# Optimization experiments

Measured on AMD Instinct MI355X. Metric: run time of the kernel, lower is better.

## Reference

```python
import jax, jax.numpy as jnp
import numpy as np

H = 64  # hidden size

def setup_inputs() -> dict:
    key = jax.random.key(0)
    ks = jax.random.split(key, 7)
    B, T = 256, 5000
    s = 1.0 / np.sqrt(H)  # PyTorch LSTM init scale
    return {
        "x":    jax.random.normal(ks[0], (B, T), dtype=jnp.float32),
        "W_ih": jax.random.uniform(ks[1], (4 * H, 1), jnp.float32, -s, s),
        "W_hh": jax.random.uniform(ks[2], (4 * H, H), jnp.float32, -s, s),
        "b_ih": jax.random.uniform(ks[3], (4 * H,), jnp.float32, -s, s),
        "b_hh": jax.random.uniform(ks[4], (4 * H,), jnp.float32, -s, s),
        "W_fc": jax.random.uniform(ks[5], (128, H), jnp.float32, -s, s),
        "b_fc": jax.random.uniform(ks[6], (128,), jnp.float32, -s, s),
    }

def _lstm_last_hidden(x, W_ih, W_hh, b_ih, b_hh):
    # x: [B, T]; returns last hidden state h_T: [B, H]
    B, T = x.shape
    # input projection for all timesteps at once: [B, T, 4H]
    # (input_size == 1, so this is an outer product with W_ih[:, 0])
    x_proj = x[:, :, None] * W_ih[:, 0][None, None, :] + (b_ih + b_hh)

    def step(carry, xp_t):
        h, c = carry
        gates = xp_t + h @ W_hh.T  # [B, 4H]
        i = jax.nn.sigmoid(gates[:, 0 * H:1 * H])
        f = jax.nn.sigmoid(gates[:, 1 * H:2 * H])
        g = jnp.tanh(gates[:, 2 * H:3 * H])
        o = jax.nn.sigmoid(gates[:, 3 * H:4 * H])
        c = f * c + i * g
        h = o * jnp.tanh(c)
        return (h, c), None

    h0 = jnp.zeros((B, H), x.dtype)
    c0 = jnp.zeros((B, H), x.dtype)
    (h, c), _ = jax.lax.scan(step, (h0, c0), jnp.swapaxes(x_proj, 0, 1))
    return h

def reference(x, W_ih, W_hh, b_ih, b_hh, W_fc, b_fc):
    h_last = _lstm_last_hidden(x, W_ih, W_hh, b_ih, b_hh)  # [B, H]
    return jax.nn.relu(h_last @ W_fc.T + b_fc)  # [B, 128]
```

## Files before the change

### kernel.cpp

```cpp
#include <hip/hip_runtime.h>


#define LSTM_H 64
#define LSTM_T 5000
#define LSTM_B 256
#define XCHUNK 256

__device__ __forceinline__ float fast_rcp(float v) {
    return __builtin_amdgcn_rcpf(v);
}

__global__ __launch_bounds__(256) void ECGLSTM_lstm_fused(
    const float* __restrict__ x,
    const float* __restrict__ W_ih,
    const float* __restrict__ W_hh,
    const float* __restrict__ b_ih,
    const float* __restrict__ b_hh,
    const float* __restrict__ W_fc,
    const float* __restrict__ b_fc,
    float* __restrict__ out)
{
    const int tid = threadIdx.x;
    const int b   = blockIdx.x;

    __shared__ float h_lds[LSTM_H];
    __shared__ float gates[4 * LSTM_H];
    __shared__ float xch[XCHUNK];

    float w[LSTM_H];
    {
        const float4* wrow = reinterpret_cast<const float4*>(W_hh + tid * LSTM_H);
        #pragma unroll
        for (int i = 0; i < LSTM_H / 4; ++i) {
            float4 v = wrow[i];
            w[4*i+0] = v.x; w[4*i+1] = v.y; w[4*i+2] = v.z; w[4*i+3] = v.w;
        }
    }
    const float wih  = W_ih[tid];
    const float bias = b_ih[tid] + b_hh[tid];
    const bool  is_tanh = ((tid >> 6) == 2);

    float c = 0.0f;
    if (tid < LSTM_H) h_lds[tid] = 0.0f;
    __syncthreads();

    const float* xb = x + b * LSTM_T;

    for (int base = 0; base < LSTM_T; base += XCHUNK) {
        const int nt = (LSTM_T - base < XCHUNK) ? (LSTM_T - base) : XCHUNK;
        if (tid < nt) xch[tid] = xb[base + tid];
        __syncthreads();

        for (int tt = 0; tt < nt; ++tt) {
            const float xv = xch[tt];

            float a0 = 0.f, a1 = 0.f, a2 = 0.f, a3 = 0.f;
            const float4* h4 = reinterpret_cast<const float4*>(h_lds);
            #pragma unroll
            for (int i = 0; i < LSTM_H / 4; ++i) {
                float4 hv = h4[i];
                a0 = fmaf(hv.x, w[4*i+0], a0);
                a1 = fmaf(hv.y, w[4*i+1], a1);
                a2 = fmaf(hv.z, w[4*i+2], a2);
                a3 = fmaf(hv.w, w[4*i+3], a3);
            }
            float g = fmaf(xv, wih, bias) + ((a0 + a1) + (a2 + a3));

            float act;
            if (is_tanh) {
                float e = __expf(2.0f * g);
                act = 1.0f - 2.0f * fast_rcp(e + 1.0f);
            } else {
                float e = __expf(-g);
                act = fast_rcp(1.0f + e);
            }
            gates[tid] = act;
            __syncthreads();

            if (tid < LSTM_H) {
                float ig = gates[tid];
                float fg = gates[LSTM_H + tid];
                float gg = gates[2 * LSTM_H + tid];
                float og = gates[3 * LSTM_H + tid];
                c = fmaf(fg, c, ig * gg);
                float e  = __expf(2.0f * c);
                float th = 1.0f - 2.0f * fast_rcp(e + 1.0f);
                h_lds[tid] = og * th;
            }
            __syncthreads();
        }
    }

    if (tid < 128) {
        float s = b_fc[tid];
        const float* wf = W_fc + tid * LSTM_H;
        #pragma unroll
        for (int k = 0; k < LSTM_H; ++k) s = fmaf(h_lds[k], wf[k], s);
        out[b * 128 + tid] = fmaxf(s, 0.0f);
    }
}

extern "C" void kernel_launch(void* const* d_in, const int* in_sizes, int n_in,
                              void* d_out, int out_size, void* d_ws, size_t ws_size,
                              hipStream_t stream) {
    const float* x    = (const float*)d_in[0];
    const float* W_ih = (const float*)d_in[1];
    const float* W_hh = (const float*)d_in[2];
    const float* b_ih = (const float*)d_in[3];
    const float* b_hh = (const float*)d_in[4];
    const float* W_fc = (const float*)d_in[5];
    const float* b_fc = (const float*)d_in[6];
    float* out = (float*)d_out;

    ECGLSTM_lstm_fused<<<LSTM_B, 256, 0, stream>>>(
        x, W_ih, W_hh, b_ih, b_hh, W_fc, b_fc, out);
}
```

Baseline: 2.487 ms.

## Replicate cell update per wave, broadcast h via readlane, single barrier per step

Every wavefront now computes the c/h update redundantly for its 64 lanes and keeps h in a register. The matvec broadcasts h through v_readlane instead of reading it from LDS. Gates are double-buffered in LDS, which removes the second __syncthreads per timestep. The x values are held in a register per 64-step chunk and read with readlane, replacing the LDS staging. This trades a barrier and LDS traffic for scalar readlane instructions, which may serialize through SGPRs, plus redundant exp work in all four waves.

```diff
diff --git a/kernel.cpp b/kernel.cpp
--- a/kernel.cpp
+++ b/kernel.cpp
@@ -4,10 +4,13 @@
 #define LSTM_H 64
 #define LSTM_T 5000
 #define LSTM_B 256
-#define XCHUNK 256
 
 __device__ __forceinline__ float fast_rcp(float v) {
     return __builtin_amdgcn_rcpf(v);
+}
+
+__device__ __forceinline__ float rl(float v, int lane) {
+    return __int_as_float(__builtin_amdgcn_readlane(__float_as_int(v), lane));
 }
 
 __global__ __launch_bounds__(256) void ECGLSTM_lstm_fused(
@@ -20,12 +23,12 @@
     const float* __restrict__ b_fc,
     float* __restrict__ out)
 {
-    const int tid = threadIdx.x;
-    const int b   = blockIdx.x;
+    const int tid  = threadIdx.x;
+    const int lane = tid & 63;
+    const int b    = blockIdx.x;
 
+    __shared__ float gates[2][4 * LSTM_H];
     __shared__ float h_lds[LSTM_H];
-    __shared__ float gates[4 * LSTM_H];
-    __shared__ float xch[XCHUNK];
 
     float w[LSTM_H];
     {
@@ -40,29 +43,27 @@
     const float bias = b_ih[tid] + b_hh[tid];
     const bool  is_tanh = ((tid >> 6) == 2);
 
+    float h = 0.0f;
     float c = 0.0f;
-    if (tid < LSTM_H) h_lds[tid] = 0.0f;
-    __syncthreads();
 
     const float* xb = x + b * LSTM_T;
 
-    for (int base = 0; base < LSTM_T; base += XCHUNK) {
-        const int nt = (LSTM_T - base < XCHUNK) ? (LSTM_T - base) : XCHUNK;
-        if (tid < nt) xch[tid] = xb[base + tid];
-        __syncthreads();
+    for (int base = 0; base < LSTM_T; base += 64) {
+        const int rem = LSTM_T - base;
+        const int nt  = rem < 64 ? rem : 64;
+        const float xreg = (lane < nt) ? xb[base + lane] : 0.0f;
 
         for (int tt = 0; tt < nt; ++tt) {
-            const float xv = xch[tt];
+            const int p = tt & 1;
+            const float xv = rl(xreg, tt);
 
             float a0 = 0.f, a1 = 0.f, a2 = 0.f, a3 = 0.f;
-            const float4* h4 = reinterpret_cast<const float4*>(h_lds);
             #pragma unroll
-            for (int i = 0; i < LSTM_H / 4; ++i) {
-                float4 hv = h4[i];
-                a0 = fmaf(hv.x, w[4*i+0], a0);
-                a1 = fmaf(hv.y, w[4*i+1], a1);
-                a2 = fmaf(hv.z, w[4*i+2], a2);
-                a3 = fmaf(hv.w, w[4*i+3], a3);
+            for (int k = 0; k < LSTM_H; k += 4) {
+                a0 = fmaf(rl(h, k + 0), w[k + 0], a0);
+                a1 = fmaf(rl(h, k + 1), w[k + 1], a1);
+                a2 = fmaf(rl(h, k + 2), w[k + 2], a2);
+                a3 = fmaf(rl(h, k + 3), w[k + 3], a3);
             }
             float g = fmaf(xv, wih, bias) + ((a0 + a1) + (a2 + a3));
 
@@ -74,28 +75,36 @@
                 float e = __expf(-g);
                 act = fast_rcp(1.0f + e);
             }
-            gates[tid] = act;
+            gates[p][tid] = act;
             __syncthreads();
 
-            if (tid < LSTM_H) {
-                float ig = gates[tid];
-                float fg = gates[LSTM_H + tid];
-                float gg = gates[2 * LSTM_H + tid];
-                float og = gates[3 * LSTM_H + tid];
-                c = fmaf(fg, c, ig * gg);
-                float e  = __expf(2.0f * c);
-                float th = 1.0f - 2.0f * fast_rcp(e + 1.0f);
-                h_lds[tid] = og * th;
-            }
-            __syncthreads();
+            const float ig = gates[p][lane];
+            const float fg = gates[p][LSTM_H + lane];
+            const float gg = gates[p][2 * LSTM_H + lane];
+            const float og = gates[p][3 * LSTM_H + lane];
+            c = fmaf(fg, c, ig * gg);
+            float e  = __expf(2.0f * c);
+            float th = 1.0f - 2.0f * fast_rcp(e + 1.0f);
+            h = og * th;
         }
     }
 
+    if (tid < LSTM_H) h_lds[tid] = h;
+    __syncthreads();
+
     if (tid < 128) {
         float s = b_fc[tid];
-        const float* wf = W_fc + tid * LSTM_H;
+        const float4* wf = reinterpret_cast<const float4*>(W_fc + tid * LSTM_H);
+        const float4* h4 = reinterpret_cast<const float4*>(h_lds);
         #pragma unroll
-        for (int k = 0; k < LSTM_H; ++k) s = fmaf(h_lds[k], wf[k], s);
+        for (int i = 0; i < LSTM_H / 4; ++i) {
+            float4 wv = wf[i];
+            float4 hv = h4[i];
+            s = fmaf(hv.x, wv.x, s);
+            s = fmaf(hv.y, wv.y, s);
+            s = fmaf(hv.z, wv.z, s);
+            s = fmaf(hv.w, wv.w, s);
+        }
         out[b * 128 + tid] = fmaxf(s, 0.0f);
     }
 }
```

Result: slower. 3.315 ms (+33.3%).
